# Kernel tuning notes

Hardware: AMD Instinct MI355X
Metric: run time of the kernel (lower is better)

## Reference

```python
import jax, jax.numpy as jnp
import numpy as np

D_MODEL = 256; N_HEADS = 8; N_LEVELS = 4; N_POINTS = 4
D_HEAD = D_MODEL // N_HEADS


def setup_inputs() -> dict:
    key = jax.random.key(0)
    ks = jax.random.split(key, 8)
    N, Lq = 4, 4096
    shapes = np.array([4096, 2048, 1024, 512], dtype=np.int32)  # temporal lengths per level
    Len_in = int(shapes.sum())  # 7680
    start = np.concatenate([[0], np.cumsum(shapes)[:-1]]).astype(np.int32)
    HLP = N_HEADS * N_LEVELS * N_POINTS
    return {
        "query": jax.random.normal(ks[0], (N, Lq, D_MODEL), jnp.float32),
        "reference_points": jax.random.uniform(ks[1], (N, Lq, N_LEVELS, 1), jnp.float32),
        "input_flatten": jax.random.normal(ks[2], (N, Len_in, D_MODEL), jnp.float32),
        "input_spatial_shapes": jnp.asarray(shapes),
        "input_level_start_index": jnp.asarray(start),
        "W_off": jax.random.normal(ks[3], (D_MODEL, HLP), jnp.float32) * 0.01,
        "b_off": jax.random.normal(ks[4], (HLP,), jnp.float32) * 2.0,
        "W_aw": jax.random.normal(ks[5], (D_MODEL, HLP), jnp.float32) * 0.02,
        "b_aw": jnp.zeros((HLP,), jnp.float32),
        "W_v": jax.random.normal(ks[6], (D_MODEL, D_MODEL), jnp.float32) / np.sqrt(D_MODEL).astype(np.float32),
        "b_v": jnp.zeros((D_MODEL,), jnp.float32),
        "W_out": jax.random.normal(ks[7], (D_MODEL, D_MODEL), jnp.float32) / np.sqrt(D_MODEL).astype(np.float32),
        "b_out": jnp.zeros((D_MODEL,), jnp.float32),
    }


def reference(query, reference_points, input_flatten, input_spatial_shapes,
              input_level_start_index, W_off, b_off, W_aw, b_aw, W_v, b_v,
              W_out, b_out):
    N, Lq, C = query.shape
    M, L, P, Dh = N_HEADS, N_LEVELS, N_POINTS, D_HEAD
    S = input_flatten.shape[1]

    value = (input_flatten @ W_v + b_v).reshape(N, S, M, Dh)
    off = (query @ W_off + b_off).reshape(N, Lq, M, L, P)
    aw = jax.nn.softmax((query @ W_aw + b_aw).reshape(N, Lq, M, L * P), axis=-1)
    aw = aw.reshape(N, Lq, M, L, P)

    # reference_points last dim == 1 branch: loc = ref + off / T_l, in [0,1]
    T = input_spatial_shapes.astype(jnp.float32)[None, None, None, :, None]  # [1,1,1,L,1]
    loc = reference_points[:, :, None, :, None, 0] + off / T  # [N,Lq,M,L,P]

    # grid_sample(align_corners=False, padding_mode='border') along W with H=1, y=0.5:
    # pixel coord x = loc*T - 0.5, clamped to [0, T-1], then linear interp.
    x = jnp.clip(loc * T - 0.5, 0.0, T - 1.0)
    x0 = jnp.floor(x)
    w1 = x - x0                                   # frac weight for right neighbor
    i0 = x0.astype(jnp.int32)
    i1 = jnp.minimum(i0 + 1, input_spatial_shapes[None, None, None, :, None] - 1)
    base = input_level_start_index[None, None, None, :, None]
    g0 = i0 + base                                # global flattened indices [N,Lq,M,L,P]
    g1 = i1 + base

    v = value.transpose(0, 2, 1, 3)               # [N,M,S,Dh]

    def gather(idx):
        idxt = idx.transpose(0, 2, 1, 3, 4).reshape(N, M, Lq * L * P, 1)
        return jnp.take_along_axis(v, idxt, axis=2).reshape(N, M, Lq, L, P, Dh)

    s0 = gather(g0)
    s1 = gather(g1)
    w1t = w1.transpose(0, 2, 1, 3, 4)[..., None]   # [N,M,Lq,L,P,1]
    samp = s0 * (1.0 - w1t) + s1 * w1t             # [N,M,Lq,L,P,Dh]

    awt = aw.transpose(0, 2, 1, 3, 4)[..., None]
    out = (samp * awt).sum(axis=(3, 4))            # [N,M,Lq,Dh]
    out = out.transpose(0, 2, 1, 3).reshape(N, Lq, M * Dh)
    return out @ W_out + b_out
```

## Files before the change

### kernel.cpp

```cpp
#include <hip/hip_runtime.h>
#include <hip/hip_bf16.h>
#include <cstddef>
#include <cstdint>

#define D_MODEL   256
#define N_HEADS   8
#define N_LEVELS  4
#define N_POINTS  4
#define D_HEAD    32
#define HLP       128
#define NBATCH    4
#define LQ        4096
#define S_LEN     7680
#define QB        4

typedef __attribute__((ext_vector_type(8))) short  short8;
typedef __attribute__((ext_vector_type(4))) float  f32x4;
typedef __attribute__((ext_vector_type(8))) unsigned short ushort8;

__device__ __forceinline__ unsigned short f2bf(float x) {
    __hip_bfloat16 h = __float2bfloat16(x);
    return *reinterpret_cast<unsigned short*>(&h);
}
__device__ __forceinline__ float bf2f(unsigned short u) {
    unsigned int v = ((unsigned int)u) << 16;
    return *reinterpret_cast<float*>(&v);
}

__device__ __forceinline__ void gload_lds16(const void* g, void* l) {
    __builtin_amdgcn_global_load_lds(
        (const __attribute__((address_space(1))) void*)g,
        (__attribute__((address_space(3))) void*)l,
        16, 0, 0);
}

__global__ __launch_bounds__(256) void prep_kernel(
    const float* __restrict__ W_v,  const float* __restrict__ W_off,
    const float* __restrict__ W_aw, const float* __restrict__ W_out,
    const float* __restrict__ b_off, const float* __restrict__ b_aw,
    unsigned short* __restrict__ Wv_t, unsigned short* __restrict__ Wcat_t,
    unsigned short* __restrict__ Wout_t, float* __restrict__ bcat)
{
    __shared__ float t[64][65];
    const int z   = blockIdx.z;
    const int k0  = blockIdx.y * 64;
    const int n0  = blockIdx.x * 64;
    const int tid = threadIdx.x;

    const float* src; int srcN; int cs; unsigned short* dst;
    if (z == 0)      { src = W_v;   srcN = 256; cs = n0;       dst = Wv_t;  }
    else if (z == 2) { src = W_out; srcN = 256; cs = n0;       dst = Wout_t;}
    else if (n0 < 128){ src = W_off; srcN = 128; cs = n0;      dst = Wcat_t;}
    else             { src = W_aw;  srcN = 128; cs = n0 - 128; dst = Wcat_t;}

    #pragma unroll
    for (int i = 0; i < 16; ++i) {
        int idx = tid + i * 256;
        int kk = idx >> 6, nn = idx & 63;
        t[kk][nn] = src[(size_t)(k0 + kk) * srcN + cs + nn];
    }
    __syncthreads();
    #pragma unroll
    for (int i = 0; i < 16; ++i) {
        int idx = tid + i * 256;
        int nn = idx >> 6, kk = idx & 63;
        dst[(size_t)(n0 + nn) * 256 + k0 + kk] = f2bf(t[kk][nn]);
    }
    if (z == 1 && blockIdx.x == 0 && blockIdx.y == 0) {
        bcat[tid] = (tid < 128) ? b_off[tid] : b_aw[tid - 128];
    }
}

__global__ __launch_bounds__(256) void gemm_vp_kernel(
    const float* __restrict__ inflat, const float* __restrict__ query,
    const unsigned short* __restrict__ Wv_t, const unsigned short* __restrict__ Wcat_t,
    const float* __restrict__ b_v, const float* __restrict__ bcat,
    unsigned short* __restrict__ value3, float* __restrict__ P)
{
    __shared__ alignas(16) unsigned short Abuf[2][8][64][8];
    __shared__ alignas(16) unsigned short Bbuf[2][8][64][8];

    const int job = blockIdx.x;
    const bool is_val = (job < 480);
    const int jj   = is_val ? job : (job - 480);
    const int row0 = (jj >> 1) * 128;
    const int col0 = (jj & 1) * 128;
    const float* A = is_val ? inflat : query;
    const unsigned short* Bt = is_val ? Wv_t : Wcat_t;
    const float* bias = is_val ? b_v : bcat;

    const int tid  = threadIdx.x;
    const int lane = tid & 63;
    const int w    = tid >> 6;
    const int wm   = w & 1;
    const int wn   = w >> 1;
    const int lr   = lane & 15;
    const int lk   = (lane >> 4) * 8;

    const float* Ap0 = A + (size_t)(row0 + (w * 2 + 0) * 16 + lr) * 256 + lk;
    const float* Ap1 = A + (size_t)(row0 + (w * 2 + 1) * 16 + lr) * 256 + lk;
    const unsigned short* Bcol = Bt + (size_t)(col0 + lr) * 256 + lk;

    f32x4 acc[4][4] = {};

    float4 a00 = *(const float4*)(Ap0), a01 = *(const float4*)(Ap0 + 4);
    float4 a10 = *(const float4*)(Ap1), a11 = *(const float4*)(Ap1 + 4);
    #pragma unroll
    for (int c = 0; c < 2; ++c) {
        const int im = w * 2 + c;
        gload_lds16(Bcol + (size_t)im * 16 * 256, &Bbuf[0][im][0][0]);
    }

    for (int kt = 0; kt < 8; ++kt) {
        const int cur = kt & 1;
        {
            short8 pk;
            pk[0] = (short)f2bf(a00.x); pk[1] = (short)f2bf(a00.y);
            pk[2] = (short)f2bf(a00.z); pk[3] = (short)f2bf(a00.w);
            pk[4] = (short)f2bf(a01.x); pk[5] = (short)f2bf(a01.y);
            pk[6] = (short)f2bf(a01.z); pk[7] = (short)f2bf(a01.w);
            *(short8*)&Abuf[cur][w * 2 + 0][lane][0] = pk;
            pk[0] = (short)f2bf(a10.x); pk[1] = (short)f2bf(a10.y);
            pk[2] = (short)f2bf(a10.z); pk[3] = (short)f2bf(a10.w);
            pk[4] = (short)f2bf(a11.x); pk[5] = (short)f2bf(a11.y);
            pk[6] = (short)f2bf(a11.z); pk[7] = (short)f2bf(a11.w);
            *(short8*)&Abuf[cur][w * 2 + 1][lane][0] = pk;
        }
        __syncthreads();

        if (kt < 7) {
            const int k1 = (kt + 1) * 32;
            a00 = *(const float4*)(Ap0 + k1); a01 = *(const float4*)(Ap0 + k1 + 4);
            a10 = *(const float4*)(Ap1 + k1); a11 = *(const float4*)(Ap1 + k1 + 4);
            #pragma unroll
            for (int c = 0; c < 2; ++c) {
                const int im = w * 2 + c;
                gload_lds16(Bcol + (size_t)im * 16 * 256 + k1, &Bbuf[1 - cur][im][0][0]);
            }
        }

        short8 af[4], bfr[4];
        #pragma unroll
        for (int i = 0; i < 4; ++i) af[i]  = *(const short8*)&Abuf[cur][wm * 4 + i][lane][0];
        #pragma unroll
        for (int j = 0; j < 4; ++j) bfr[j] = *(const short8*)&Bbuf[cur][wn * 4 + j][lane][0];

        #pragma unroll
        for (int i = 0; i < 4; ++i)
            #pragma unroll
            for (int j = 0; j < 4; ++j)
                acc[i][j] = __builtin_amdgcn_mfma_f32_16x16x32_bf16(
                    af[i], bfr[j], acc[i][j], 0, 0, 0);
    }

    const int prow = (lane >> 4) * 4;
    const int pcol = lane & 15;
    if (is_val) {
        const int n  = row0 / S_LEN;
        const int s0 = row0 - n * S_LEN + wm * 64;
        #pragma unroll
        for (int j = 0; j < 4; ++j) {
            const int col = col0 + wn * 64 + j * 16 + pcol;
            const float bs = bias[col];
            const int m = col >> 5, d = col & 31;
            unsigned short* dst = value3 + ((size_t)(n * 8 + m) * S_LEN + s0) * 32 + d;
            #pragma unroll
            for (int i = 0; i < 4; ++i) {
                #pragma unroll
                for (int r = 0; r < 4; ++r) {
                    const int rl = i * 16 + prow + r;
                    dst[(size_t)rl * 32] = f2bf(acc[i][j][r] + bs);
                }
            }
        }
    } else {
        #pragma unroll
        for (int j = 0; j < 4; ++j) {
            const int col = col0 + wn * 64 + j * 16 + pcol;
            const float bs = bias[col];
            #pragma unroll
            for (int i = 0; i < 4; ++i) {
                #pragma unroll
                for (int r = 0; r < 4; ++r) {
                    const int row = row0 + wm * 64 + i * 16 + prow + r;
                    P[(size_t)row * 256 + col] = acc[i][j][r] + bs;
                }
            }
        }
    }
}

__global__ __launch_bounds__(128) void sample_kernel(
    const float* __restrict__ P, const float* __restrict__ refp,
    const int* __restrict__ shapes, const int* __restrict__ lstart,
    const unsigned short* __restrict__ value3,
    unsigned short* __restrict__ tout)
{
    __shared__ int   sG0[QB][130];
    __shared__ float sW [QB][130];
    __shared__ float sA [QB][130];
    __shared__ int   glim[4];

    const int b    = blockIdx.x;
    const int xcd  = b & 7;
    const int n    = xcd >> 1;
    const int half = xcd & 1;
    const int slot = b >> 3;
    const int q0   = (slot * 2 + half) * QB;
    const int nq0  = n * LQ + q0;
    const int tid  = threadIdx.x;

    if (tid < 4) glim[tid] = lstart[tid] + shapes[tid] - 1;

    #pragma unroll
    for (int it = 0; it < 4; ++it) {
        const int idx = tid + it * 128;
        const int q   = idx >> 7;
        const int j   = idx & 127;
        const int l   = (j >> 2) & 3;
        const int nq  = nq0 + q;
        const float off   = __builtin_nontemporal_load(P + (size_t)nq * 256 + j);
        const float logit = __builtin_nontemporal_load(P + (size_t)nq * 256 + 128 + j);
        const float ref   = __builtin_nontemporal_load(refp + (size_t)nq * N_LEVELS + l);
        const int   sh    = shapes[l];
        const float Tf    = (float)sh;
        float x = ref * Tf + off - 0.5f;
        x = fminf(fmaxf(x, 0.0f), Tf - 1.0f);
        const float x0 = floorf(x);
        sG0[q][j] = (int)x0 + lstart[l];
        sW [q][j] = x - x0;
        sA [q][j] = logit;
    }
    __syncthreads();

    const int q  = tid >> 5;
    const int r  = tid & 31;
    const int m  = r >> 2;
    const int ql = r & 3;
    const unsigned short* vb =
        value3 + (size_t)(n * 8 + m) * S_LEN * 32 + ql * 8;

    float e[16];
    float mx = -1e30f;
    #pragma unroll
    for (int i = 0; i < 16; ++i) { e[i] = sA[q][m * 16 + i]; mx = fmaxf(mx, e[i]); }
    float s = 0.f;
    #pragma unroll
    for (int i = 0; i < 16; ++i) { e[i] = __expf(e[i] - mx); s += e[i]; }
    const float rs = 1.0f / s;

    float acc[8] = {};
    #pragma unroll
    for (int c = 0; c < 4; ++c) {
        ushort8 u0[4], u1[4];
        float   aw[4], wl[4];
        #pragma unroll
        for (int i4 = 0; i4 < 4; ++i4) {
            const int i = c * 4 + i4;
            const int j = m * 16 + i;
            aw[i4] = e[i] * rs;
            wl[i4] = sW[q][j];
            const int g0 = sG0[q][j];
            const int g1 = min(g0 + 1, glim[i >> 2]);
            u0[i4] = *(const ushort8*)(vb + (size_t)g0 * 32);
            u1[i4] = *(const ushort8*)(vb + (size_t)g1 * 32);
        }
        #pragma unroll
        for (int i4 = 0; i4 < 4; ++i4) {
            #pragma unroll
            for (int d = 0; d < 8; ++d) {
                const float v0 = bf2f(u0[i4][d]);
                const float v1 = bf2f(u1[i4][d]);
                acc[d] += aw[i4] * (v0 + wl[i4] * (v1 - v0));
            }
        }
    }
    ushort8 o;
    #pragma unroll
    for (int d = 0; d < 8; ++d) o[d] = f2bf(acc[d]);
    __builtin_nontemporal_store(o,
        (ushort8*)(tout + (size_t)(nq0 + q) * 256 + m * 32 + ql * 8));
}

__global__ __launch_bounds__(256) void gemm_out_kernel(
    const unsigned short* __restrict__ A,
    const unsigned short* __restrict__ Bt,
    const float* __restrict__ bias,
    float* __restrict__ Cout)
{
    __shared__ alignas(16) unsigned short Abuf[2][4][64][8];
    __shared__ alignas(16) unsigned short Bbuf[2][8][64][8];

    const int jj   = blockIdx.x;
    const int row0 = (jj >> 1) * 64;
    const int col0 = (jj & 1) * 128;

    const int tid  = threadIdx.x;
    const int lane = tid & 63;
    const int w    = tid >> 6;
    const int wm   = w & 1;
    const int wn   = w >> 1;
    const int lr   = lane & 15;
    const int lk   = (lane >> 4) * 8;

    const unsigned short* Arow = A + (size_t)(row0 + w * 16 + lr) * 256 + lk;
    const unsigned short* Bcol = Bt + (size_t)(col0 + lr) * 256 + lk;

    f32x4 acc[2][4] = {};

    gload_lds16(Arow, &Abuf[0][w][0][0]);
    #pragma unroll
    for (int c = 0; c < 2; ++c) {
        const int im = w * 2 + c;
        gload_lds16(Bcol + (size_t)im * 16 * 256, &Bbuf[0][im][0][0]);
    }

    for (int kt = 0; kt < 8; ++kt) {
        const int cur = kt & 1;
        __syncthreads();

        if (kt < 7) {
            const int k1 = (kt + 1) * 32;
            gload_lds16(Arow + k1, &Abuf[1 - cur][w][0][0]);
            #pragma unroll
            for (int c = 0; c < 2; ++c) {
                const int im = w * 2 + c;
                gload_lds16(Bcol + (size_t)im * 16 * 256 + k1, &Bbuf[1 - cur][im][0][0]);
            }
        }

        short8 af[2], bfr[4];
        #pragma unroll
        for (int i = 0; i < 2; ++i) af[i]  = *(const short8*)&Abuf[cur][wm * 2 + i][lane][0];
        #pragma unroll
        for (int j = 0; j < 4; ++j) bfr[j] = *(const short8*)&Bbuf[cur][wn * 4 + j][lane][0];

        #pragma unroll
        for (int i = 0; i < 2; ++i)
            #pragma unroll
            for (int j = 0; j < 4; ++j)
                acc[i][j] = __builtin_amdgcn_mfma_f32_16x16x32_bf16(
                    af[i], bfr[j], acc[i][j], 0, 0, 0);
    }

    const int prow = (lane >> 4) * 4;
    const int pcol = lane & 15;
    #pragma unroll
    for (int i = 0; i < 2; ++i) {
        #pragma unroll
        for (int j = 0; j < 4; ++j) {
            const int col = col0 + wn * 64 + j * 16 + pcol;
            const float bs = bias[col];
            const int rbase = row0 + wm * 32 + i * 16 + prow;
            #pragma unroll
            for (int r = 0; r < 4; ++r)
                Cout[(size_t)(rbase + r) * 256 + col] = acc[i][j][r] + bs;
        }
    }
}

extern "C" void kernel_launch(void* const* d_in, const int* in_sizes, int n_in,
                              void* d_out, int out_size, void* d_ws, size_t ws_size,
                              hipStream_t stream)
{
    const float* query  = (const float*)d_in[0];
    const float* refp   = (const float*)d_in[1];
    const float* inflat = (const float*)d_in[2];
    const int*   shapes = (const int*)d_in[3];
    const int*   lstart = (const int*)d_in[4];
    const float* W_off  = (const float*)d_in[5];
    const float* b_off  = (const float*)d_in[6];
    const float* W_aw   = (const float*)d_in[7];
    const float* b_aw   = (const float*)d_in[8];
    const float* W_v    = (const float*)d_in[9];
    const float* b_v    = (const float*)d_in[10];
    const float* W_out  = (const float*)d_in[11];
    const float* b_out  = (const float*)d_in[12];

    const int M_val = NBATCH * S_LEN;
    const int M_q   = NBATCH * LQ;

    char* p = (char*)d_ws;
    unsigned short* value3 = (unsigned short*)p; p += (size_t)M_val * D_MODEL * 2;
    float*          P      = (float*)p;          p += (size_t)M_q * 256 * 4;
    unsigned short* tbuf   = (unsigned short*)p; p += (size_t)M_q * D_MODEL * 2;
    unsigned short* Wv_t   = (unsigned short*)p; p += 256 * 256 * 2;
    unsigned short* Wcat_t = (unsigned short*)p; p += 256 * 256 * 2;
    unsigned short* Wout_t = (unsigned short*)p; p += 256 * 256 * 2;
    float*          bcat   = (float*)p;          p += 256 * 4;

    prep_kernel<<<dim3(4, 4, 3), 256, 0, stream>>>(
        W_v, W_off, W_aw, W_out, b_off, b_aw, Wv_t, Wcat_t, Wout_t, bcat);
    gemm_vp_kernel<<<736, 256, 0, stream>>>(
        inflat, query, Wv_t, Wcat_t, b_v, bcat, value3, P);
    sample_kernel<<<4096, 128, 0, stream>>>(
        P, refp, shapes, lstart, value3, tbuf);
    gemm_out_kernel<<<512, 256, 0, stream>>>(
        tbuf, Wout_t, b_out, (float*)d_out);
}
```

Before: 168.2 us.

## Replace LDS-staged block GEMMs with per-wave register-only 64x64 tile GEMMs

Both projection GEMMs and the output GEMM now have each wave compute an independent 64x64 tile. The wave loads A and B fragments directly from global memory into registers, double-buffered across k-steps. This removes LDS staging, global_load_lds and block barriers. In exchange, data reuse across waves in a block is lost: B and A tiles are reloaded per wave through cache, and register pressure rises from the extra prefetch buffers.

```diff
diff --git a/kernel.cpp b/kernel.cpp
--- a/kernel.cpp
+++ b/kernel.cpp
@@ -27,13 +27,6 @@
     return *reinterpret_cast<float*>(&v);
 }
 
-__device__ __forceinline__ void gload_lds16(const void* g, void* l) {
-    __builtin_amdgcn_global_load_lds(
-        (const __attribute__((address_space(1))) void*)g,
-        (__attribute__((address_space(3))) void*)l,
-        16, 0, 0);
-}
-
 __global__ __launch_bounds__(256) void prep_kernel(
     const float* __restrict__ W_v,  const float* __restrict__ W_off,
     const float* __restrict__ W_aw, const float* __restrict__ W_out,
@@ -71,122 +64,152 @@
     }
 }
 
+template <bool A_FP32>
+__device__ __forceinline__ void wave_gemm64(
+    const void* __restrict__ Aptr, const unsigned short* __restrict__ Bt,
+    int row0, int col0, int lane, f32x4 acc[4][4])
+{
+    const int lr = lane & 15;
+    const int lk = (lane >> 4) * 8;
+
+    const float*          Afp[4];
+    const unsigned short* Abf[4];
+    const unsigned short* Bp[4];
+    #pragma unroll
+    for (int i = 0; i < 4; ++i) {
+        if (A_FP32) Afp[i] = (const float*)Aptr + (size_t)(row0 + i * 16 + lr) * 256 + lk;
+        else        Abf[i] = (const unsigned short*)Aptr + (size_t)(row0 + i * 16 + lr) * 256 + lk;
+        Bp[i] = Bt + (size_t)(col0 + i * 16 + lr) * 256 + lk;
+    }
+
+    float4  raf[4][2]; short8 rab[4];
+    short8  rb[4];
+    float4  naf[4][2]; short8 nab[4];
+    short8  nb[4];
+
+    #pragma unroll
+    for (int i = 0; i < 4; ++i) {
+        if (A_FP32) { raf[i][0] = *(const float4*)(Afp[i]); raf[i][1] = *(const float4*)(Afp[i] + 4); }
+        else        { rab[i] = *(const short8*)(Abf[i]); }
+        rb[i] = *(const short8*)(Bp[i]);
+    }
+
+    #pragma unroll
+    for (int kt = 0; kt < 8; ++kt) {
+        if (kt < 7) {
+            const int k1 = (kt + 1) * 32;
+            #pragma unroll
+            for (int i = 0; i < 4; ++i) {
+                if (A_FP32) { naf[i][0] = *(const float4*)(Afp[i] + k1); naf[i][1] = *(const float4*)(Afp[i] + k1 + 4); }
+                else        { nab[i] = *(const short8*)(Abf[i] + k1); }
+                nb[i] = *(const short8*)(Bp[i] + k1);
+            }
+        }
+        short8 af[4];
+        #pragma unroll
+        for (int i = 0; i < 4; ++i) {
+            if (A_FP32) {
+                short8 pk;
+                pk[0] = (short)f2bf(raf[i][0].x); pk[1] = (short)f2bf(raf[i][0].y);
+                pk[2] = (short)f2bf(raf[i][0].z); pk[3] = (short)f2bf(raf[i][0].w);
+                pk[4] = (short)f2bf(raf[i][1].x); pk[5] = (short)f2bf(raf[i][1].y);
+                pk[6] = (short)f2bf(raf[i][1].z); pk[7] = (short)f2bf(raf[i][1].w);
+                af[i] = pk;
+            } else {
+                af[i] = rab[i];
+            }
+        }
+        #pragma unroll
+        for (int i = 0; i < 4; ++i)
+            #pragma unroll
+            for (int j = 0; j < 4; ++j)
+                acc[i][j] = __builtin_amdgcn_mfma_f32_16x16x32_bf16(
+                    af[i], rb[j], acc[i][j], 0, 0, 0);
+        if (kt < 7) {
+            #pragma unroll
+            for (int i = 0; i < 4; ++i) {
+                if (A_FP32) { raf[i][0] = naf[i][0]; raf[i][1] = naf[i][1]; }
+                else        { rab[i] = nab[i]; }
+                rb[i] = nb[i];
+            }
+        }
+    }
+}
+
 __global__ __launch_bounds__(256) void gemm_vp_kernel(
     const float* __restrict__ inflat, const float* __restrict__ query,
     const unsigned short* __restrict__ Wv_t, const unsigned short* __restrict__ Wcat_t,
     const float* __restrict__ b_v, const float* __restrict__ bcat,
     unsigned short* __restrict__ value3, float* __restrict__ P)
 {
-    __shared__ alignas(16) unsigned short Abuf[2][8][64][8];
-    __shared__ alignas(16) unsigned short Bbuf[2][8][64][8];
-
-    const int job = blockIdx.x;
-    const bool is_val = (job < 480);
-    const int jj   = is_val ? job : (job - 480);
-    const int row0 = (jj >> 1) * 128;
-    const int col0 = (jj & 1) * 128;
-    const float* A = is_val ? inflat : query;
-    const unsigned short* Bt = is_val ? Wv_t : Wcat_t;
+    const int wave = (blockIdx.x << 2) | (threadIdx.x >> 6);
+    const int lane = threadIdx.x & 63;
+    const bool is_val = (wave < 1920);
+    const int jj   = is_val ? wave : (wave - 1920);
+    const int row0 = (jj >> 2) * 64;
+    const int col0 = (jj & 3) * 64;
+
+    f32x4 acc[4][4] = {};
+    wave_gemm64<true>(is_val ? (const void*)inflat : (const void*)query,
+                      is_val ? Wv_t : Wcat_t, row0, col0, lane, acc);
+
     const float* bias = is_val ? b_v : bcat;
-
-    const int tid  = threadIdx.x;
-    const int lane = tid & 63;
-    const int w    = tid >> 6;
-    const int wm   = w & 1;
-    const int wn   = w >> 1;
-    const int lr   = lane & 15;
-    const int lk   = (lane >> 4) * 8;
-
-    const float* Ap0 = A + (size_t)(row0 + (w * 2 + 0) * 16 + lr) * 256 + lk;
-    const float* Ap1 = A + (size_t)(row0 + (w * 2 + 1) * 16 + lr) * 256 + lk;
-    const unsigned short* Bcol = Bt + (size_t)(col0 + lr) * 256 + lk;
-
-    f32x4 acc[4][4] = {};
-
-    float4 a00 = *(const float4*)(Ap0), a01 = *(const float4*)(Ap0 + 4);
-    float4 a10 = *(const float4*)(Ap1), a11 = *(const float4*)(Ap1 + 4);
-    #pragma unroll
-    for (int c = 0; c < 2; ++c) {
-        const int im = w * 2 + c;
-        gload_lds16(Bcol + (size_t)im * 16 * 256, &Bbuf[0][im][0][0]);
-    }
-
-    for (int kt = 0; kt < 8; ++kt) {
-        const int cur = kt & 1;
-        {
-            short8 pk;
-            pk[0] = (short)f2bf(a00.x); pk[1] = (short)f2bf(a00.y);
-            pk[2] = (short)f2bf(a00.z); pk[3] = (short)f2bf(a00.w);
-            pk[4] = (short)f2bf(a01.x); pk[5] = (short)f2bf(a01.y);
-            pk[6] = (short)f2bf(a01.z); pk[7] = (short)f2bf(a01.w);
-            *(short8*)&Abuf[cur][w * 2 + 0][lane][0] = pk;
-            pk[0] = (short)f2bf(a10.x); pk[1] = (short)f2bf(a10.y);
-            pk[2] = (short)f2bf(a10.z); pk[3] = (short)f2bf(a10.w);
-            pk[4] = (short)f2bf(a11.x); pk[5] = (short)f2bf(a11.y);
-            pk[6] = (short)f2bf(a11.z); pk[7] = (short)f2bf(a11.w);
-            *(short8*)&Abuf[cur][w * 2 + 1][lane][0] = pk;
-        }
-        __syncthreads();
-
-        if (kt < 7) {
-            const int k1 = (kt + 1) * 32;
-            a00 = *(const float4*)(Ap0 + k1); a01 = *(const float4*)(Ap0 + k1 + 4);
-            a10 = *(const float4*)(Ap1 + k1); a11 = *(const float4*)(Ap1 + k1 + 4);
-            #pragma unroll
-            for (int c = 0; c < 2; ++c) {
-                const int im = w * 2 + c;
-                gload_lds16(Bcol + (size_t)im * 16 * 256 + k1, &Bbuf[1 - cur][im][0][0]);
-            }
-        }
-
-        short8 af[4], bfr[4];
-        #pragma unroll
-        for (int i = 0; i < 4; ++i) af[i]  = *(const short8*)&Abuf[cur][wm * 4 + i][lane][0];
-        #pragma unroll
-        for (int j = 0; j < 4; ++j) bfr[j] = *(const short8*)&Bbuf[cur][wn * 4 + j][lane][0];
-
-        #pragma unroll
-        for (int i = 0; i < 4; ++i)
-            #pragma unroll
-            for (int j = 0; j < 4; ++j)
-                acc[i][j] = __builtin_amdgcn_mfma_f32_16x16x32_bf16(
-                    af[i], bfr[j], acc[i][j], 0, 0, 0);
-    }
-
     const int prow = (lane >> 4) * 4;
     const int pcol = lane & 15;
     if (is_val) {
         const int n  = row0 / S_LEN;
-        const int s0 = row0 - n * S_LEN + wm * 64;
+        const int s0 = row0 - n * S_LEN;
         #pragma unroll
         for (int j = 0; j < 4; ++j) {
-            const int col = col0 + wn * 64 + j * 16 + pcol;
+            const int col = col0 + j * 16 + pcol;
             const float bs = bias[col];
             const int m = col >> 5, d = col & 31;
             unsigned short* dst = value3 + ((size_t)(n * 8 + m) * S_LEN + s0) * 32 + d;
             #pragma unroll
-            for (int i = 0; i < 4; ++i) {
+            for (int i = 0; i < 4; ++i)
                 #pragma unroll
-                for (int r = 0; r < 4; ++r) {
-                    const int rl = i * 16 + prow + r;
-                    dst[(size_t)rl * 32] = f2bf(acc[i][j][r] + bs);
-                }
-            }
+                for (int r = 0; r < 4; ++r)
+                    dst[(size_t)(i * 16 + prow + r) * 32] = f2bf(acc[i][j][r] + bs);
         }
     } else {
         #pragma unroll
         for (int j = 0; j < 4; ++j) {
-            const int col = col0 + wn * 64 + j * 16 + pcol;
+            const int col = col0 + j * 16 + pcol;
             const float bs = bias[col];
             #pragma unroll
-            for (int i = 0; i < 4; ++i) {
+            for (int i = 0; i < 4; ++i)
                 #pragma unroll
-                for (int r = 0; r < 4; ++r) {
-                    const int row = row0 + wm * 64 + i * 16 + prow + r;
-                    P[(size_t)row * 256 + col] = acc[i][j][r] + bs;
-                }
-            }
-        }
+                for (int r = 0; r < 4; ++r)
+                    P[(size_t)(row0 + i * 16 + prow + r) * 256 + col] = acc[i][j][r] + bs;
+        }
+    }
+}
+
+__global__ __launch_bounds__(256) void gemm_out_kernel(
+    const unsigned short* __restrict__ A,
+    const unsigned short* __restrict__ Bt,
+    const float* __restrict__ bias,
+    float* __restrict__ Cout)
+{
+    const int wave = (blockIdx.x << 2) | (threadIdx.x >> 6);
+    const int lane = threadIdx.x & 63;
+    const int row0 = (wave >> 2) * 64;
+    const int col0 = (wave & 3) * 64;
+
+    f32x4 acc[4][4] = {};
+    wave_gemm64<false>(A, Bt, row0, col0, lane, acc);
+
+    const int prow = (lane >> 4) * 4;
+    const int pcol = lane & 15;
+    #pragma unroll
+    for (int j = 0; j < 4; ++j) {
+        const int col = col0 + j * 16 + pcol;
+        const float bs = bias[col];
+        #pragma unroll
+        for (int i = 0; i < 4; ++i)
+            #pragma unroll
+            for (int r = 0; r < 4; ++r)
+                Cout[(size_t)(row0 + i * 16 + prow + r) * 256 + col] = acc[i][j][r] + bs;
     }
 }
 
@@ -282,83 +305,6 @@
         (ushort8*)(tout + (size_t)(nq0 + q) * 256 + m * 32 + ql * 8));
 }
 
-__global__ __launch_bounds__(256) void gemm_out_kernel(
-    const unsigned short* __restrict__ A,
-    const unsigned short* __restrict__ Bt,
-    const float* __restrict__ bias,
-    float* __restrict__ Cout)
-{
-    __shared__ alignas(16) unsigned short Abuf[2][4][64][8];
-    __shared__ alignas(16) unsigned short Bbuf[2][8][64][8];
-
-    const int jj   = blockIdx.x;
-    const int row0 = (jj >> 1) * 64;
-    const int col0 = (jj & 1) * 128;
-
-    const int tid  = threadIdx.x;
-    const int lane = tid & 63;
-    const int w    = tid >> 6;
-    const int wm   = w & 1;
-    const int wn   = w >> 1;
-    const int lr   = lane & 15;
-    const int lk   = (lane >> 4) * 8;
-
-    const unsigned short* Arow = A + (size_t)(row0 + w * 16 + lr) * 256 + lk;
-    const unsigned short* Bcol = Bt + (size_t)(col0 + lr) * 256 + lk;
-
-    f32x4 acc[2][4] = {};
-
-    gload_lds16(Arow, &Abuf[0][w][0][0]);
-    #pragma unroll
-    for (int c = 0; c < 2; ++c) {
-        const int im = w * 2 + c;
-        gload_lds16(Bcol + (size_t)im * 16 * 256, &Bbuf[0][im][0][0]);
-    }
-
-    for (int kt = 0; kt < 8; ++kt) {
-        const int cur = kt & 1;
-        __syncthreads();
-
-        if (kt < 7) {
-            const int k1 = (kt + 1) * 32;
-            gload_lds16(Arow + k1, &Abuf[1 - cur][w][0][0]);
-            #pragma unroll
-            for (int c = 0; c < 2; ++c) {
-                const int im = w * 2 + c;
-                gload_lds16(Bcol + (size_t)im * 16 * 256 + k1, &Bbuf[1 - cur][im][0][0]);
-            }
-        }
-
-        short8 af[2], bfr[4];
-        #pragma unroll
-        for (int i = 0; i < 2; ++i) af[i]  = *(const short8*)&Abuf[cur][wm * 2 + i][lane][0];
-        #pragma unroll
-        for (int j = 0; j < 4; ++j) bfr[j] = *(const short8*)&Bbuf[cur][wn * 4 + j][lane][0];
-
-        #pragma unroll
-        for (int i = 0; i < 2; ++i)
-            #pragma unroll
-            for (int j = 0; j < 4; ++j)
-                acc[i][j] = __builtin_amdgcn_mfma_f32_16x16x32_bf16(
-                    af[i], bfr[j], acc[i][j], 0, 0, 0);
-    }
-
-    const int prow = (lane >> 4) * 4;
-    const int pcol = lane & 15;
-    #pragma unroll
-    for (int i = 0; i < 2; ++i) {
-        #pragma unroll
-        for (int j = 0; j < 4; ++j) {
-            const int col = col0 + wn * 64 + j * 16 + pcol;
-            const float bs = bias[col];
-            const int rbase = row0 + wm * 32 + i * 16 + prow;
-            #pragma unroll
-            for (int r = 0; r < 4; ++r)
-                Cout[(size_t)(rbase + r) * 256 + col] = acc[i][j][r] + bs;
-        }
-    }
-}
-
 extern "C" void kernel_launch(void* const* d_in, const int* in_sizes, int n_in,
                               void* d_out, int out_size, void* d_ws, size_t ws_size,
                               hipStream_t stream)
@@ -395,6 +341,6 @@
         inflat, query, Wv_t, Wcat_t, b_v, bcat, value3, P);
     sample_kernel<<<4096, 128, 0, stream>>>(
         P, refp, shapes, lstart, value3, tbuf);
-    gemm_out_kernel<<<512, 256, 0, stream>>>(
+    gemm_out_kernel<<<256, 256, 0, stream>>>(
         tbuf, Wout_t, b_out, (float*)d_out);
 }
```

Measured after the change: 174.6 us. +3.8%, slower.
